# Optimization experiments

Hardware: AMD Instinct MI355X
Metric: run time of the kernel (lower is better)

## Reference

```python
import jax, jax.numpy as jnp
import numpy as np

NUM_HEADS = 8
LN_EPS = 1e-8


def setup_inputs() -> dict:
    key = jax.random.key(0)
    ks = jax.random.split(key, 10)
    B, Sq, Sk, D, U = 8, 1024, 1024, 512, 512
    s = 1.0 / np.sqrt(D)
    return {
        "queries": jax.random.normal(ks[0], (B, Sq, D), jnp.float32),
        "keys": jax.random.normal(ks[1], (B, Sk, D), jnp.float32),
        "Wq": jax.random.normal(ks[2], (D, U), jnp.float32) * s,
        "bq": jnp.zeros((U,), jnp.float32),
        "Wk": jax.random.normal(ks[3], (D, U), jnp.float32) * s,
        "bk": jnp.zeros((U,), jnp.float32),
        "Wv": jax.random.normal(ks[4], (D, U), jnp.float32) * s,
        "bv": jnp.zeros((U,), jnp.float32),
        "gamma": jnp.ones((U,), jnp.float32),
        "beta": jnp.zeros((U,), jnp.float32),
    }


def reference(queries, keys, Wq, bq, Wk, bk, Wv, bv, gamma, beta):
    H = NUM_HEADS
    B, Sq, _ = queries.shape
    Sk = keys.shape[1]
    U = Wq.shape[1]
    Dh = U // H

    # ReLU-activated Q/K/V projections
    Q = jax.nn.relu(queries @ Wq + bq)   # [B,Sq,U]
    K = jax.nn.relu(keys @ Wk + bk)      # [B,Sk,U]
    V = jax.nn.relu(keys @ Wv + bv)      # [B,Sk,U]

    # split_heads: concat(split(x, H, -1), 0) == head-major [H,B,S,Dh]
    Qh = Q.reshape(B, Sq, H, Dh).transpose(2, 0, 1, 3)
    Kh = K.reshape(B, Sk, H, Dh).transpose(2, 0, 1, 3)
    Vh = V.reshape(B, Sk, H, Dh).transpose(2, 0, 1, 3)

    scores = jnp.einsum('hbqd,hbkd->hbqk', Qh, Kh) / jnp.sqrt(
        jnp.asarray(Dh, scores_dtype := Qh.dtype))
    attn = jax.nn.softmax(scores, axis=-1)

    # post-softmax query mask: zero rows where sum(|q|)==0 ([B,Sq,1] bcast)
    qmask = (jnp.sum(jnp.abs(queries), axis=-1, keepdims=True) > 0)
    attn = attn * qmask.astype(attn.dtype)[None]  # [1,B,Sq,1] -> [H,B,Sq,Sk]

    out = jnp.einsum('hbqk,hbkd->hbqd', attn, Vh)  # [H,B,Sq,Dh]
    # merge_heads: inverse of split_heads
    out = out.transpose(1, 2, 0, 3).reshape(B, Sq, U)

    out = out + queries  # residual

    # LayerNorm over last axis (keras default), eps=1e-8
    mu = jnp.mean(out, axis=-1, keepdims=True)
    var = jnp.mean(jnp.square(out - mu), axis=-1, keepdims=True)
    return gamma * (out - mu) * jax.lax.rsqrt(var + LN_EPS) + beta
```

## Files before the change

### kernel.cpp

```cpp
#include <hip/hip_runtime.h>
#include <stdint.h>

#define ROWS 8192
#define UDIM 512
#define SEQ  1024
#define NH   8
#define DH   64
#define SCALE 0.125f
#define LOG2E 1.44269504f
#define SC_Q (SCALE * LOG2E)

typedef unsigned short u16;
typedef __bf16 bf16_t;
typedef bf16_t bf16x8 __attribute__((ext_vector_type(8)));
typedef float f32x4 __attribute__((ext_vector_type(4)));

__device__ __forceinline__ u16 f2bf(float f) {
    union { float f; uint32_t u; } v; v.f = f;
    uint32_t r = v.u + 0x7FFFu + ((v.u >> 16) & 1u);
    return (u16)(r >> 16);
}

__device__ __forceinline__ uint32_t pk_bf16(float a, float b) {
#if __has_builtin(__builtin_amdgcn_cvt_pk_bf16_f32)
    typedef __bf16 bf16x2_t __attribute__((ext_vector_type(2)));
    bf16x2_t r = __builtin_amdgcn_cvt_pk_bf16_f32(a, b);
    union { bf16x2_t v; uint32_t u; } c; c.v = r;
    return c.u;
#else
    return (uint32_t)f2bf(a) | ((uint32_t)f2bf(b) << 16);
#endif
}

__device__ __forceinline__ void async_ld16(u16* lds, const u16* g) {
    __builtin_amdgcn_global_load_lds((const __attribute__((address_space(1))) void*)g,
                                     (__attribute__((address_space(3))) void*)lds, 16, 0, 0);
}

__global__ void convqk_kernel(const float* __restrict__ q, const float* __restrict__ k,
                              u16* __restrict__ qb, u16* __restrict__ kb,
                              float* __restrict__ qmask) {
    int w = threadIdx.x >> 6, lane = threadIdx.x & 63;
    int row = blockIdx.x * 4 + w;
    const float* src = (blockIdx.y == 0) ? q : k;
    u16* dst = (blockIdx.y == 0) ? qb : kb;
    const float4* s4 = (const float4*)(src + (size_t)row * UDIM);
    ushort4* o4 = (ushort4*)(dst + (size_t)row * UDIM);
    float s = 0.f;
    for (int j = 0; j < 2; j++) {
        float4 v = s4[j * 64 + lane];
        s += fabsf(v.x) + fabsf(v.y) + fabsf(v.z) + fabsf(v.w);
        ushort4 b;
        b.x = f2bf(v.x); b.y = f2bf(v.y); b.z = f2bf(v.z); b.w = f2bf(v.w);
        o4[j * 64 + lane] = b;
    }
    if (blockIdx.y == 0) {
        for (int off = 32; off; off >>= 1) s += __shfl_xor(s, off, 64);
        if (lane == 0) qmask[row] = (s > 0.f) ? 1.f : 0.f;
    }
}

__global__ void transposeW_kernel(const float* __restrict__ Wq, const float* __restrict__ Wk,
                                  const float* __restrict__ Wv, u16* __restrict__ Wqt,
                                  u16* __restrict__ Wkt, u16* __restrict__ Wvt) {
    const float* in = (blockIdx.z == 0) ? Wq : (blockIdx.z == 1) ? Wk : Wv;
    u16* out = (blockIdx.z == 0) ? Wqt : (blockIdx.z == 1) ? Wkt : Wvt;
    __shared__ float tile[32][33];
    int k0 = blockIdx.y * 32, n0 = blockIdx.x * 32;
    int tx = threadIdx.x & 31, ty = threadIdx.x >> 5;
    for (int r = ty; r < 32; r += 8)
        tile[r][tx] = in[(size_t)(k0 + r) * UDIM + n0 + tx];
    __syncthreads();
    for (int r = ty; r < 32; r += 8)
        out[(size_t)(n0 + r) * UDIM + k0 + tx] = f2bf(tile[tx][r]);
}

__global__ __launch_bounds__(256, 3) void proj_kernel(
    const u16* __restrict__ qb, const u16* __restrict__ kb,
    const u16* __restrict__ Wqt, const u16* __restrict__ Wkt, const u16* __restrict__ Wvt,
    const float* __restrict__ bq, const float* __restrict__ bk, const float* __restrict__ bv,
    u16* __restrict__ Qp, u16* __restrict__ Kp, u16* __restrict__ Vtp)
{
    const int z = blockIdx.z;
    const u16* A = (z == 0) ? qb : kb;
    const u16* W = (z == 0) ? Wqt : (z == 1) ? Wkt : Wvt;
    const float* bias = (z == 0) ? bq : (z == 1) ? bk : bv;

    __shared__ u16 a_s[128 * 32];
    __shared__ u16 b_s[128 * 32];

    const int t = threadIdx.x;
    const int lane = t & 63, w = t >> 6;
    const int quad = lane >> 4, l15 = lane & 15;
    const int m0 = blockIdx.x * 128;
    const int n0 = blockIdx.y * 128;

    f32x4 acc[2][8];
    for (int mi = 0; mi < 2; mi++)
        for (int ni = 0; ni < 8; ni++)
            acc[mi][ni] = (f32x4){0.f, 0.f, 0.f, 0.f};

    for (int kt = 0; kt < 512; kt += 32) {
        for (int rnd = 0; rnd < 2; rnd++) {
            int c = t + rnd * 256;
            int row = c >> 2;
            int jg = (c & 3) ^ ((row >> 1) & 3);
            async_ld16(&a_s[c * 8], &A[(size_t)(m0 + row) * 512 + kt + jg * 8]);
            async_ld16(&b_s[c * 8], &W[(size_t)(n0 + row) * 512 + kt + jg * 8]);
        }
        __syncthreads();
        bf16x8 af[2], bf[8];
        for (int mi = 0; mi < 2; mi++) {
            int row = w * 32 + mi * 16 + l15;
            int ps = quad ^ ((row >> 1) & 3);
            af[mi] = *(const bf16x8*)&a_s[row * 32 + ps * 8];
        }
        for (int ni = 0; ni < 8; ni++) {
            int row = ni * 16 + l15;
            int ps = quad ^ ((row >> 1) & 3);
            bf[ni] = *(const bf16x8*)&b_s[row * 32 + ps * 8];
        }
        for (int mi = 0; mi < 2; mi++)
            for (int ni = 0; ni < 8; ni++)
                acc[mi][ni] = __builtin_amdgcn_mfma_f32_16x16x32_bf16(af[mi], bf[ni], acc[mi][ni], 0, 0, 0);
        __syncthreads();
    }

    const float qscale = (z == 0) ? SC_Q : 1.f;
    for (int mi = 0; mi < 2; mi++) {
        for (int ni = 0; ni < 8; ni++) {
            int gn = n0 + ni * 16 + l15;
            float bvl = bias[gn];
            if (z < 2) {
                u16* outp = (z == 0) ? Qp : Kp;
                for (int r = 0; r < 4; r++) {
                    int gm = m0 + w * 32 + mi * 16 + quad * 4 + r;
                    float v = fmaxf(acc[mi][ni][r] + bvl, 0.f) * qscale;
                    outp[(size_t)gm * 512 + gn] = f2bf(v);
                }
            } else {
                int gmb = m0 + w * 32 + mi * 16 + quad * 4;
                int b = gmb >> 10;
                int sk = gmb & 1023;
                float v0 = fmaxf(acc[mi][ni][0] + bvl, 0.f);
                float v1 = fmaxf(acc[mi][ni][1] + bvl, 0.f);
                float v2 = fmaxf(acc[mi][ni][2] + bvl, 0.f);
                float v3 = fmaxf(acc[mi][ni][3] + bvl, 0.f);
                uint2 pk;
                pk.x = pk_bf16(v0, v1);
                pk.y = pk_bf16(v2, v3);
                *(uint2*)&Vtp[(size_t)(b * 512 + gn) * 1024 + sk] = pk;
            }
        }
    }
}

__global__ __launch_bounds__(256, 4) void attn_kernel(
    const u16* __restrict__ Qb, const u16* __restrict__ Kb, const u16* __restrict__ Vt,
    float* __restrict__ O)
{
    __shared__ u16 q_s[64 * 64];
    __shared__ u16 k_s[64 * 64];
    __shared__ u16 v_s[64 * 64];
    __shared__ u16 p_s[64 * 64];

    const int t = threadIdx.x, lane = t & 63, w = t >> 6;
    const int quad = lane >> 4, l15 = lane & 15;
    const int fid = blockIdx.x;
    const int xcd = fid & 7, j = fid >> 3;
    const int hb = xcd * 8 + (j & 7);
    const int qt = j >> 3;
    const int h = hb & 7, b = hb >> 3;
    const int q0 = qt * 64;

    for (int rnd = 0; rnd < 2; rnd++) {
        int c = t + rnd * 256;
        int row = c >> 3;
        int jg = (c & 7) ^ (row & 7);
        async_ld16(&q_s[c * 8], &Qb[(size_t)(b * 1024 + q0 + row) * 512 + h * 64 + jg * 8]);
    }
    __syncthreads();

    bf16x8 bqf[2];
    {
        int row = w * 16 + l15;
        for (int kk = 0; kk < 2; kk++) {
            int ps = (kk * 4 + quad) ^ (row & 7);
            bqf[kk] = *(const bf16x8*)&q_s[row * 64 + ps * 8];
        }
    }

    float l_lane = 0.f;
    f32x4 o_acc[4];
    for (int mi = 0; mi < 4; mi++) o_acc[mi] = (f32x4){0.f, 0.f, 0.f, 0.f};

    for (int kv0 = 0; kv0 < 1024; kv0 += 64) {
        for (int rnd = 0; rnd < 2; rnd++) {
            int c = t + rnd * 256;
            int row = c >> 3;
            int jg = (c & 7) ^ (row & 7);
            async_ld16(&k_s[c * 8], &Kb[(size_t)(b * 1024 + kv0 + row) * 512 + h * 64 + jg * 8]);
            async_ld16(&v_s[c * 8], &Vt[(size_t)(b * 512 + h * 64 + row) * 1024 + kv0 + jg * 8]);
        }
        __syncthreads();

        f32x4 st[4];
        for (int mi = 0; mi < 4; mi++) {
            int row = mi * 16 + l15;
            int p0 = quad ^ (row & 7);
            int p1 = (4 + quad) ^ (row & 7);
            bf16x8 ak0 = *(const bf16x8*)&k_s[row * 64 + p0 * 8];
            bf16x8 ak1 = *(const bf16x8*)&k_s[row * 64 + 32 + (p1 - 4) * 8];
            f32x4 a = (f32x4){0.f, 0.f, 0.f, 0.f};
            a = __builtin_amdgcn_mfma_f32_16x16x32_bf16(ak0, bqf[0], a, 0, 0, 0);
            a = __builtin_amdgcn_mfma_f32_16x16x32_bf16(ak1, bqf[1], a, 0, 0, 0);
            st[mi] = a;
        }

        int prow = w * 16 + l15;
        for (int mi = 0; mi < 4; mi++) {
            float p0 = exp2f(st[mi][0]);
            float p1 = exp2f(st[mi][1]);
            float p2 = exp2f(st[mi][2]);
            float p3 = exp2f(st[mi][3]);
            l_lane += (p0 + p1) + (p2 + p3);
            int psl = (mi * 2 + (quad >> 1)) ^ (prow & 7);
            uint2 pk;
            pk.x = pk_bf16(p0, p1);
            pk.y = pk_bf16(p2, p3);
            *(uint2*)&p_s[prow * 64 + psl * 8 + (quad & 1) * 4] = pk;
        }

        for (int kk = 0; kk < 2; kk++) {
            int pp = (kk * 4 + quad) ^ (prow & 7);
            bf16x8 bp = *(const bf16x8*)&p_s[prow * 64 + pp * 8];
            for (int mi = 0; mi < 4; mi++) {
                int vrow = mi * 16 + l15;
                int vp = (kk * 4 + quad) ^ (vrow & 7);
                bf16x8 av = *(const bf16x8*)&v_s[vrow * 64 + vp * 8];
                o_acc[mi] = __builtin_amdgcn_mfma_f32_16x16x32_bf16(av, bp, o_acc[mi], 0, 0, 0);
            }
        }
        __syncthreads();
    }

    float l = l_lane;
    l += __shfl_xor(l, 16, 64);
    l += __shfl_xor(l, 32, 64);
    float inv = 1.f / l;

    int gq = q0 + w * 16 + l15;
    for (int mi = 0; mi < 4; mi++) {
        float4 o;
        o.x = o_acc[mi][0] * inv;
        o.y = o_acc[mi][1] * inv;
        o.z = o_acc[mi][2] * inv;
        o.w = o_acc[mi][3] * inv;
        *(float4*)&O[(size_t)(b * 1024 + gq) * 512 + h * 64 + mi * 16 + quad * 4] = o;
    }
}

__global__ void ln_kernel(const float* __restrict__ O, const float* __restrict__ q,
                          const float* __restrict__ qmask, const float* __restrict__ gamma,
                          const float* __restrict__ beta, float* __restrict__ out)
{
    int w = threadIdx.x >> 6, lane = threadIdx.x & 63;
    int row = blockIdx.x * 4 + w;
    const float4* O4 = (const float4*)(O + (size_t)row * UDIM);
    const float4* q4 = (const float4*)(q + (size_t)row * UDIM);
    float4* o4 = (float4*)(out + (size_t)row * UDIM);
    float mask = qmask[row];
    float4 x[2];
    float s = 0.f, ss = 0.f;
    for (int j = 0; j < 2; j++) {
        float4 a = O4[j * 64 + lane], qq = q4[j * 64 + lane];
        float4 v;
        v.x = a.x * mask + qq.x;
        v.y = a.y * mask + qq.y;
        v.z = a.z * mask + qq.z;
        v.w = a.w * mask + qq.w;
        x[j] = v;
        s += v.x + v.y + v.z + v.w;
        ss += v.x * v.x + v.y * v.y + v.z * v.z + v.w * v.w;
    }
    for (int off = 32; off; off >>= 1) {
        s += __shfl_xor(s, off, 64);
        ss += __shfl_xor(ss, off, 64);
    }
    float mu = s * (1.f / 512.f);
    float var = ss * (1.f / 512.f) - mu * mu;
    float rs = rsqrtf(var + 1e-8f);
    for (int j = 0; j < 2; j++) {
        float4 g = ((const float4*)gamma)[j * 64 + lane];
        float4 bb = ((const float4*)beta)[j * 64 + lane];
        float4 v;
        v.x = g.x * (x[j].x - mu) * rs + bb.x;
        v.y = g.y * (x[j].y - mu) * rs + bb.y;
        v.z = g.z * (x[j].z - mu) * rs + bb.z;
        v.w = g.w * (x[j].w - mu) * rs + bb.w;
        o4[j * 64 + lane] = v;
    }
}

extern "C" void kernel_launch(void* const* d_in, const int* in_sizes, int n_in,
                              void* d_out, int out_size, void* d_ws, size_t ws_size,
                              hipStream_t stream)
{
    const float* queries = (const float*)d_in[0];
    const float* keys    = (const float*)d_in[1];
    const float* Wq      = (const float*)d_in[2];
    const float* bq      = (const float*)d_in[3];
    const float* Wk      = (const float*)d_in[4];
    const float* bk      = (const float*)d_in[5];
    const float* Wv      = (const float*)d_in[6];
    const float* bv      = (const float*)d_in[7];
    const float* gamma   = (const float*)d_in[8];
    const float* beta    = (const float*)d_in[9];
    float* out = (float*)d_out;

    char* ws = (char*)d_ws;
    size_t off = 0;
    auto alloc = [&](size_t bytes) {
        void* p = ws + off;
        off += (bytes + 255) & ~(size_t)255;
        return p;
    };
    u16* qb   = (u16*)alloc((size_t)ROWS * UDIM * 2);
    u16* kb   = (u16*)alloc((size_t)ROWS * UDIM * 2);
    u16* Wqt  = (u16*)alloc((size_t)UDIM * UDIM * 2);
    u16* Wkt  = (u16*)alloc((size_t)UDIM * UDIM * 2);
    u16* Wvt  = (u16*)alloc((size_t)UDIM * UDIM * 2);
    u16* Qp   = (u16*)alloc((size_t)ROWS * UDIM * 2);
    u16* Kp   = (u16*)alloc((size_t)ROWS * UDIM * 2);
    u16* Vtp  = (u16*)alloc((size_t)ROWS * UDIM * 2);
    float* Of = (float*)alloc((size_t)ROWS * UDIM * 4);
    float* qm = (float*)alloc((size_t)ROWS * 4);

    convqk_kernel<<<dim3(ROWS / 4, 2), 256, 0, stream>>>(queries, keys, qb, kb, qm);
    transposeW_kernel<<<dim3(16, 16, 3), 256, 0, stream>>>(Wq, Wk, Wv, Wqt, Wkt, Wvt);
    proj_kernel<<<dim3(64, 4, 3), 256, 0, stream>>>(qb, kb, Wqt, Wkt, Wvt, bq, bk, bv, Qp, Kp, Vtp);
    attn_kernel<<<1024, 256, 0, stream>>>(Qp, Kp, Vtp, Of);
    ln_kernel<<<ROWS / 4, 256, 0, stream>>>(Of, queries, qm, gamma, beta, out);
}
```

Baseline: 163.8 us.

## Stage projection epilogue through LDS, precompute LDS offsets, move qmask into LN

The projection epilogue now writes bias+ReLU results into a padded shared-memory tile and stores them to global memory as coalesced 16-byte rows, for both Q/K and the transposed V output. This replaces scattered 2-byte and 8-byte stores. The GEMM and attention inner loops use precomputed swizzled LDS offsets and incrementing global pointers, which removes per-iteration index arithmetic. The query mask is now computed inside the layernorm kernel from the query row it already loads, so the separate mask buffer and its reduction in the conversion kernel go away. The LDS footprint grows to the padded C tile, which could affect occupancy.

```diff
diff --git a/kernel.cpp b/kernel.cpp
--- a/kernel.cpp
+++ b/kernel.cpp
@@ -38,25 +38,18 @@
 }
 
 __global__ void convqk_kernel(const float* __restrict__ q, const float* __restrict__ k,
-                              u16* __restrict__ qb, u16* __restrict__ kb,
-                              float* __restrict__ qmask) {
+                              u16* __restrict__ qb, u16* __restrict__ kb) {
     int w = threadIdx.x >> 6, lane = threadIdx.x & 63;
     int row = blockIdx.x * 4 + w;
     const float* src = (blockIdx.y == 0) ? q : k;
     u16* dst = (blockIdx.y == 0) ? qb : kb;
     const float4* s4 = (const float4*)(src + (size_t)row * UDIM);
     ushort4* o4 = (ushort4*)(dst + (size_t)row * UDIM);
-    float s = 0.f;
     for (int j = 0; j < 2; j++) {
         float4 v = s4[j * 64 + lane];
-        s += fabsf(v.x) + fabsf(v.y) + fabsf(v.z) + fabsf(v.w);
         ushort4 b;
         b.x = f2bf(v.x); b.y = f2bf(v.y); b.z = f2bf(v.z); b.w = f2bf(v.w);
         o4[j * 64 + lane] = b;
-    }
-    if (blockIdx.y == 0) {
-        for (int off = 32; off; off >>= 1) s += __shfl_xor(s, off, 64);
-        if (lane == 0) qmask[row] = (s > 0.f) ? 1.f : 0.f;
     }
 }
 
@@ -75,6 +68,7 @@
         out[(size_t)(n0 + r) * UDIM + k0 + tx] = f2bf(tile[tx][r]);
 }
 
+#define CPAD 136
 __global__ __launch_bounds__(256, 3) void proj_kernel(
     const u16* __restrict__ qb, const u16* __restrict__ kb,
     const u16* __restrict__ Wqt, const u16* __restrict__ Wkt, const u16* __restrict__ Wvt,
@@ -86,8 +80,10 @@
     const u16* W = (z == 0) ? Wqt : (z == 1) ? Wkt : Wvt;
     const float* bias = (z == 0) ? bq : (z == 1) ? bk : bv;
 
-    __shared__ u16 a_s[128 * 32];
-    __shared__ u16 b_s[128 * 32];
+    __shared__ u16 smem[128 * CPAD];
+    u16* a_s = smem;
+    u16* b_s = smem + 4096;
+    u16* c_s = smem;
 
     const int t = threadIdx.x;
     const int lane = t & 63, w = t >> 6;
@@ -95,31 +91,38 @@
     const int m0 = blockIdx.x * 128;
     const int n0 = blockIdx.y * 128;
 
+    const int r0 = t >> 2;
+    const int s0 = ((t & 3) ^ ((r0 >> 1) & 3)) * 8;
+    const u16* Ag0 = &A[(size_t)(m0 + r0) * 512 + s0];
+    const u16* Ag1 = Ag0 + (size_t)64 * 512;
+    const u16* Wg0 = &W[(size_t)(n0 + r0) * 512 + s0];
+    const u16* Wg1 = Wg0 + (size_t)64 * 512;
+    u16* al0 = &a_s[t * 8];       u16* al1 = &a_s[(t + 256) * 8];
+    u16* bl0 = &b_s[t * 8];       u16* bl1 = &b_s[(t + 256) * 8];
+
+    int aoff[2], boff[8];
+    for (int mi = 0; mi < 2; mi++) {
+        int row = w * 32 + mi * 16 + l15;
+        aoff[mi] = row * 32 + (quad ^ ((row >> 1) & 3)) * 8;
+    }
+    for (int ni = 0; ni < 8; ni++) {
+        int row = ni * 16 + l15;
+        boff[ni] = row * 32 + (quad ^ ((row >> 1) & 3)) * 8;
+    }
+
     f32x4 acc[2][8];
     for (int mi = 0; mi < 2; mi++)
         for (int ni = 0; ni < 8; ni++)
             acc[mi][ni] = (f32x4){0.f, 0.f, 0.f, 0.f};
 
     for (int kt = 0; kt < 512; kt += 32) {
-        for (int rnd = 0; rnd < 2; rnd++) {
-            int c = t + rnd * 256;
-            int row = c >> 2;
-            int jg = (c & 3) ^ ((row >> 1) & 3);
-            async_ld16(&a_s[c * 8], &A[(size_t)(m0 + row) * 512 + kt + jg * 8]);
-            async_ld16(&b_s[c * 8], &W[(size_t)(n0 + row) * 512 + kt + jg * 8]);
-        }
+        async_ld16(al0, Ag0);  async_ld16(al1, Ag1);
+        async_ld16(bl0, Wg0);  async_ld16(bl1, Wg1);
+        Ag0 += 32; Ag1 += 32; Wg0 += 32; Wg1 += 32;
         __syncthreads();
         bf16x8 af[2], bf[8];
-        for (int mi = 0; mi < 2; mi++) {
-            int row = w * 32 + mi * 16 + l15;
-            int ps = quad ^ ((row >> 1) & 3);
-            af[mi] = *(const bf16x8*)&a_s[row * 32 + ps * 8];
-        }
-        for (int ni = 0; ni < 8; ni++) {
-            int row = ni * 16 + l15;
-            int ps = quad ^ ((row >> 1) & 3);
-            bf[ni] = *(const bf16x8*)&b_s[row * 32 + ps * 8];
-        }
+        for (int mi = 0; mi < 2; mi++) af[mi] = *(const bf16x8*)&a_s[aoff[mi]];
+        for (int ni = 0; ni < 8; ni++) bf[ni] = *(const bf16x8*)&b_s[boff[ni]];
         for (int mi = 0; mi < 2; mi++)
             for (int ni = 0; ni < 8; ni++)
                 acc[mi][ni] = __builtin_amdgcn_mfma_f32_16x16x32_bf16(af[mi], bf[ni], acc[mi][ni], 0, 0, 0);
@@ -127,30 +130,42 @@
     }
 
     const float qscale = (z == 0) ? SC_Q : 1.f;
-    for (int mi = 0; mi < 2; mi++) {
-        for (int ni = 0; ni < 8; ni++) {
-            int gn = n0 + ni * 16 + l15;
-            float bvl = bias[gn];
-            if (z < 2) {
-                u16* outp = (z == 0) ? Qp : Kp;
-                for (int r = 0; r < 4; r++) {
-                    int gm = m0 + w * 32 + mi * 16 + quad * 4 + r;
-                    float v = fmaxf(acc[mi][ni][r] + bvl, 0.f) * qscale;
-                    outp[(size_t)gm * 512 + gn] = f2bf(v);
-                }
-            } else {
-                int gmb = m0 + w * 32 + mi * 16 + quad * 4;
-                int b = gmb >> 10;
-                int sk = gmb & 1023;
-                float v0 = fmaxf(acc[mi][ni][0] + bvl, 0.f);
-                float v1 = fmaxf(acc[mi][ni][1] + bvl, 0.f);
-                float v2 = fmaxf(acc[mi][ni][2] + bvl, 0.f);
-                float v3 = fmaxf(acc[mi][ni][3] + bvl, 0.f);
+    float bvl[8];
+    for (int ni = 0; ni < 8; ni++) bvl[ni] = bias[n0 + ni * 16 + l15];
+    for (int mi = 0; mi < 2; mi++)
+        for (int ni = 0; ni < 8; ni++)
+            for (int r = 0; r < 4; r++)
+                acc[mi][ni][r] = fmaxf(acc[mi][ni][r] + bvl[ni], 0.f) * qscale;
+
+    if (z < 2) {
+        for (int mi = 0; mi < 2; mi++)
+            for (int ni = 0; ni < 8; ni++)
+                for (int r = 0; r < 4; r++)
+                    c_s[(w * 32 + mi * 16 + quad * 4 + r) * CPAD + ni * 16 + l15] =
+                        f2bf(acc[mi][ni][r]);
+        __syncthreads();
+        u16* outp = (z == 0) ? Qp : Kp;
+        for (int j = 0; j < 8; j++) {
+            int c = t + j * 256;
+            int mrow = c >> 4, col8 = c & 15;
+            uint4 d = *(const uint4*)&c_s[mrow * CPAD + col8 * 8];
+            *(uint4*)&outp[(size_t)(m0 + mrow) * 512 + n0 + col8 * 8] = d;
+        }
+    } else {
+        for (int mi = 0; mi < 2; mi++)
+            for (int ni = 0; ni < 8; ni++) {
                 uint2 pk;
-                pk.x = pk_bf16(v0, v1);
-                pk.y = pk_bf16(v2, v3);
-                *(uint2*)&Vtp[(size_t)(b * 512 + gn) * 1024 + sk] = pk;
+                pk.x = pk_bf16(acc[mi][ni][0], acc[mi][ni][1]);
+                pk.y = pk_bf16(acc[mi][ni][2], acc[mi][ni][3]);
+                *(uint2*)&c_s[(ni * 16 + l15) * CPAD + w * 32 + mi * 16 + quad * 4] = pk;
             }
+        __syncthreads();
+        const int bb = m0 >> 10, sk0 = m0 & 1023;
+        for (int j = 0; j < 8; j++) {
+            int c = t + j * 256;
+            int nrow = c >> 4, col8 = c & 15;
+            uint4 d = *(const uint4*)&c_s[nrow * CPAD + col8 * 8];
+            *(uint4*)&Vtp[(size_t)(bb * 512 + n0 + nrow) * 1024 + sk0 + col8 * 8] = d;
         }
     }
 }
@@ -173,83 +188,85 @@
     const int h = hb & 7, b = hb >> 3;
     const int q0 = qt * 64;
 
-    for (int rnd = 0; rnd < 2; rnd++) {
-        int c = t + rnd * 256;
-        int row = c >> 3;
-        int jg = (c & 7) ^ (row & 7);
-        async_ld16(&q_s[c * 8], &Qb[(size_t)(b * 1024 + q0 + row) * 512 + h * 64 + jg * 8]);
-    }
+    const int r0 = t >> 3;
+    const int s0 = ((t & 7) ^ (r0 & 7)) * 8;
+    u16* kl0 = &k_s[t * 8];       u16* kl1 = &k_s[(t + 256) * 8];
+    u16* vl0 = &v_s[t * 8];       u16* vl1 = &v_s[(t + 256) * 8];
+    const u16* kg0 = &Kb[(size_t)(b * 1024 + r0) * 512 + h * 64 + s0];
+    const u16* kg1 = kg0 + (size_t)32 * 512;
+    const u16* vg0 = &Vt[(size_t)(b * 512 + h * 64 + r0) * 1024 + s0];
+    const u16* vg1 = vg0 + (size_t)32 * 1024;
+
+    async_ld16(&q_s[t * 8],        &Qb[(size_t)(b * 1024 + q0 + r0) * 512 + h * 64 + s0]);
+    async_ld16(&q_s[(t + 256) * 8], &Qb[(size_t)(b * 1024 + q0 + 32 + r0) * 512 + h * 64 + s0]);
     __syncthreads();
 
+    const int prow = w * 16 + l15;
     bf16x8 bqf[2];
-    {
-        int row = w * 16 + l15;
-        for (int kk = 0; kk < 2; kk++) {
-            int ps = (kk * 4 + quad) ^ (row & 7);
-            bqf[kk] = *(const bf16x8*)&q_s[row * 64 + ps * 8];
-        }
-    }
-
-    float l_lane = 0.f;
+    for (int kk = 0; kk < 2; kk++)
+        bqf[kk] = *(const bf16x8*)&q_s[prow * 64 + ((kk * 4 + quad) ^ (prow & 7)) * 8];
+
+    int koff[4][2], voff[2][4], pwoff[4], proff[2];
+    for (int mi = 0; mi < 4; mi++) {
+        int row = mi * 16 + l15;
+        koff[mi][0] = row * 64 + (quad ^ (row & 7)) * 8;
+        koff[mi][1] = row * 64 + ((4 + quad) ^ (row & 7)) * 8;
+        voff[0][mi] = row * 64 + (quad ^ (row & 7)) * 8;
+        voff[1][mi] = row * 64 + ((4 + quad) ^ (row & 7)) * 8;
+        pwoff[mi] = prow * 64 + ((mi * 2 + (quad >> 1)) ^ (prow & 7)) * 8 + (quad & 1) * 4;
+    }
+    for (int kk = 0; kk < 2; kk++)
+        proff[kk] = prow * 64 + ((kk * 4 + quad) ^ (prow & 7)) * 8;
+
+    float l4[4] = {0.f, 0.f, 0.f, 0.f};
     f32x4 o_acc[4];
     for (int mi = 0; mi < 4; mi++) o_acc[mi] = (f32x4){0.f, 0.f, 0.f, 0.f};
 
-    for (int kv0 = 0; kv0 < 1024; kv0 += 64) {
-        for (int rnd = 0; rnd < 2; rnd++) {
-            int c = t + rnd * 256;
-            int row = c >> 3;
-            int jg = (c & 7) ^ (row & 7);
-            async_ld16(&k_s[c * 8], &Kb[(size_t)(b * 1024 + kv0 + row) * 512 + h * 64 + jg * 8]);
-            async_ld16(&v_s[c * 8], &Vt[(size_t)(b * 512 + h * 64 + row) * 1024 + kv0 + jg * 8]);
-        }
+    for (int it = 0; it < 16; it++) {
+        async_ld16(kl0, kg0);  async_ld16(kl1, kg1);
+        async_ld16(vl0, vg0);  async_ld16(vl1, vg1);
+        kg0 += (size_t)64 * 512; kg1 += (size_t)64 * 512;
+        vg0 += 64; vg1 += 64;
         __syncthreads();
 
         f32x4 st[4];
         for (int mi = 0; mi < 4; mi++) {
-            int row = mi * 16 + l15;
-            int p0 = quad ^ (row & 7);
-            int p1 = (4 + quad) ^ (row & 7);
-            bf16x8 ak0 = *(const bf16x8*)&k_s[row * 64 + p0 * 8];
-            bf16x8 ak1 = *(const bf16x8*)&k_s[row * 64 + 32 + (p1 - 4) * 8];
+            bf16x8 ak0 = *(const bf16x8*)&k_s[koff[mi][0]];
+            bf16x8 ak1 = *(const bf16x8*)&k_s[koff[mi][1]];
             f32x4 a = (f32x4){0.f, 0.f, 0.f, 0.f};
             a = __builtin_amdgcn_mfma_f32_16x16x32_bf16(ak0, bqf[0], a, 0, 0, 0);
             a = __builtin_amdgcn_mfma_f32_16x16x32_bf16(ak1, bqf[1], a, 0, 0, 0);
             st[mi] = a;
         }
 
-        int prow = w * 16 + l15;
         for (int mi = 0; mi < 4; mi++) {
             float p0 = exp2f(st[mi][0]);
             float p1 = exp2f(st[mi][1]);
             float p2 = exp2f(st[mi][2]);
             float p3 = exp2f(st[mi][3]);
-            l_lane += (p0 + p1) + (p2 + p3);
-            int psl = (mi * 2 + (quad >> 1)) ^ (prow & 7);
+            l4[mi] += (p0 + p1) + (p2 + p3);
             uint2 pk;
             pk.x = pk_bf16(p0, p1);
             pk.y = pk_bf16(p2, p3);
-            *(uint2*)&p_s[prow * 64 + psl * 8 + (quad & 1) * 4] = pk;
+            *(uint2*)&p_s[pwoff[mi]] = pk;
         }
 
         for (int kk = 0; kk < 2; kk++) {
-            int pp = (kk * 4 + quad) ^ (prow & 7);
-            bf16x8 bp = *(const bf16x8*)&p_s[prow * 64 + pp * 8];
+            bf16x8 bp = *(const bf16x8*)&p_s[proff[kk]];
             for (int mi = 0; mi < 4; mi++) {
-                int vrow = mi * 16 + l15;
-                int vp = (kk * 4 + quad) ^ (vrow & 7);
-                bf16x8 av = *(const bf16x8*)&v_s[vrow * 64 + vp * 8];
+                bf16x8 av = *(const bf16x8*)&v_s[voff[kk][mi]];
                 o_acc[mi] = __builtin_amdgcn_mfma_f32_16x16x32_bf16(av, bp, o_acc[mi], 0, 0, 0);
             }
         }
         __syncthreads();
     }
 
-    float l = l_lane;
+    float l = (l4[0] + l4[1]) + (l4[2] + l4[3]);
     l += __shfl_xor(l, 16, 64);
     l += __shfl_xor(l, 32, 64);
     float inv = 1.f / l;
 
-    int gq = q0 + w * 16 + l15;
+    int gq = q0 + prow;
     for (int mi = 0; mi < 4; mi++) {
         float4 o;
         o.x = o_acc[mi][0] * inv;
@@ -261,24 +278,33 @@
 }
 
 __global__ void ln_kernel(const float* __restrict__ O, const float* __restrict__ q,
-                          const float* __restrict__ qmask, const float* __restrict__ gamma,
-                          const float* __restrict__ beta, float* __restrict__ out)
+                          const float* __restrict__ gamma, const float* __restrict__ beta,
+                          float* __restrict__ out)
 {
     int w = threadIdx.x >> 6, lane = threadIdx.x & 63;
     int row = blockIdx.x * 4 + w;
     const float4* O4 = (const float4*)(O + (size_t)row * UDIM);
     const float4* q4 = (const float4*)(q + (size_t)row * UDIM);
     float4* o4 = (float4*)(out + (size_t)row * UDIM);
-    float mask = qmask[row];
+
+    float4 qq[2], oo[2];
+    float am = 0.f;
+    for (int j = 0; j < 2; j++) {
+        qq[j] = q4[j * 64 + lane];
+        oo[j] = O4[j * 64 + lane];
+        am += fabsf(qq[j].x) + fabsf(qq[j].y) + fabsf(qq[j].z) + fabsf(qq[j].w);
+    }
+    for (int off = 32; off; off >>= 1) am += __shfl_xor(am, off, 64);
+    float mask = (am > 0.f) ? 1.f : 0.f;
+
     float4 x[2];
     float s = 0.f, ss = 0.f;
     for (int j = 0; j < 2; j++) {
-        float4 a = O4[j * 64 + lane], qq = q4[j * 64 + lane];
         float4 v;
-        v.x = a.x * mask + qq.x;
-        v.y = a.y * mask + qq.y;
-        v.z = a.z * mask + qq.z;
-        v.w = a.w * mask + qq.w;
+        v.x = oo[j].x * mask + qq[j].x;
+        v.y = oo[j].y * mask + qq[j].y;
+        v.z = oo[j].z * mask + qq[j].z;
+        v.w = oo[j].w * mask + qq[j].w;
         x[j] = v;
         s += v.x + v.y + v.z + v.w;
         ss += v.x * v.x + v.y * v.y + v.z * v.z + v.w * v.w;
@@ -334,11 +360,10 @@
     u16* Kp   = (u16*)alloc((size_t)ROWS * UDIM * 2);
     u16* Vtp  = (u16*)alloc((size_t)ROWS * UDIM * 2);
     float* Of = (float*)alloc((size_t)ROWS * UDIM * 4);
-    float* qm = (float*)alloc((size_t)ROWS * 4);
-
-    convqk_kernel<<<dim3(ROWS / 4, 2), 256, 0, stream>>>(queries, keys, qb, kb, qm);
+
+    convqk_kernel<<<dim3(ROWS / 4, 2), 256, 0, stream>>>(queries, keys, qb, kb);
     transposeW_kernel<<<dim3(16, 16, 3), 256, 0, stream>>>(Wq, Wk, Wv, Wqt, Wkt, Wvt);
     proj_kernel<<<dim3(64, 4, 3), 256, 0, stream>>>(qb, kb, Wqt, Wkt, Wvt, bq, bk, bv, Qp, Kp, Vtp);
     attn_kernel<<<1024, 256, 0, stream>>>(Qp, Kp, Vtp, Of);
-    ln_kernel<<<ROWS / 4, 256, 0, stream>>>(Of, queries, qm, gamma, beta, out);
-}
+    ln_kernel<<<ROWS / 4, 256, 0, stream>>>(Of, queries, gamma, beta, out);
+}
```

After: 161.8 us. About the same (-1.2%).
